# Performance work log

Measured on AMD Instinct MI355X. Metric: run time of the kernel, lower is better.

Reference implementation:

```python
import jax, jax.numpy as jnp
import numpy as np
import math

N, E, C, H = 16384, 8192, 256, 8
NNZ = 262144  # incidence pairs, avg vertex degree 16


def setup_inputs() -> dict:
    key = jax.random.key(0)
    ks = jax.random.split(key, 12)
    s = 1.0 / math.sqrt(C)
    inp = {
        "X": jax.random.normal(ks[0], (N, C), dtype=jnp.float32),
        "v_ids": jax.random.randint(ks[1], (NNZ,), 0, N, dtype=jnp.int32),
        "e_ids": jax.random.randint(ks[2], (NNZ,), 0, E, dtype=jnp.int32),
        # Linear params stored as [in, out]; y = x @ W + b  (matches torch x @ W.T + b)
        "Wq": jax.random.uniform(ks[3], (C, C), jnp.float32, -s, s),
        "bq": jax.random.uniform(ks[4], (C,), jnp.float32, -s, s),
        "Wk": jax.random.uniform(ks[5], (C, C), jnp.float32, -s, s),
        "bk": jax.random.uniform(ks[6], (C,), jnp.float32, -s, s),
        "Wv": jax.random.uniform(ks[7], (C, C), jnp.float32, -s, s),
        "bv": jax.random.uniform(ks[8], (C,), jnp.float32, -s, s),
        "Wke": jax.random.uniform(ks[9], (C, C), jnp.float32, -s, s),
        "bke": jax.random.uniform(ks[10], (C,), jnp.float32, -s, s),
    }
    return inp


def reference(X, v_ids, e_ids, Wq, bq, Wk, bk, Wv, bv, Wke, bke):
    d = C // H
    scale = 1.0 / math.sqrt(d)

    Q = (X @ Wq + bq).reshape(N, H, d)
    K = (X @ Wk + bk).reshape(N, H, d)
    V = (X @ Wv + bv).reshape(N, H, d)

    # hg.v2e_aggregation(X, 'mean'): segment-mean of incident vertex features per hyperedge
    sums = jax.ops.segment_sum(X[v_ids], e_ids, num_segments=E)          # [E, C]
    cnt = jax.ops.segment_sum(jnp.ones((NNZ,), X.dtype), e_ids, num_segments=E)
    Xe = sums / jnp.maximum(cnt, 1.0)[:, None]                            # [E, C]

    Ke = Xe @ Wke + bke                                                   # [E, C]
    Qe = X @ Wq + bq                                                      # [N, C]

    # per-node attention over heads: [N, H, H]
    attn_n = jax.nn.softmax(jnp.einsum('nhd,ngd->nhg', Q, K) * scale, axis=-1)
    X_node = jnp.einsum('nhg,ngd->nhd', attn_n, V).reshape(N, C)          # [N, C]

    # node -> hyperedge attention: [N, E]
    attn_e = jax.nn.softmax((Qe @ Ke.T) * scale, axis=-1)
    X_hyperedge = attn_e @ Xe                                             # [N, C]

    out = X_node + X_hyperedge
    # is_last=False: ReLU; bn=None; dropout in eval mode (identity)
    return jax.nn.relu(out)
```

## Files before the change

### kernel.cpp

```cpp
#include <hip/hip_runtime.h>

typedef unsigned short u16;
typedef unsigned int u32;
typedef __attribute__((ext_vector_type(4))) float f32x4;
typedef __attribute__((ext_vector_type(16))) float f32x16;
typedef __attribute__((ext_vector_type(8))) short bf16x8;
typedef __attribute__((ext_vector_type(4))) short bf16x4;
typedef __attribute__((ext_vector_type(4))) u16 u16x4;

#define N_NODES 16384
#define N_EDGES 8192
#define FK_SCALE 0.17677669529663687f
#define LOG2E 1.4426950408889634f
#define C1EXP (FK_SCALE * LOG2E)
#define NSPLIT 2

typedef const u32 __attribute__((address_space(1))) gu32;
typedef u32 __attribute__((address_space(3))) lu32;

__device__ __forceinline__ void gl_lds16(const void* g, void* l) {
  __builtin_amdgcn_global_load_lds((gu32*)g, (lu32*)l, 16, 0, 0);
}

__device__ __forceinline__ float b2f(u16 u) {
  return __builtin_bit_cast(float, (u32)u << 16);
}
__device__ __forceinline__ u16 f2b(float f) {
  u32 u = __builtin_bit_cast(u32, f);
  u += 0x7fffu + ((u >> 16) & 1u);
  return (u16)(u >> 16);
}

__global__ __launch_bounds__(256) void k_cvt(const float* __restrict__ X,
                                             u16* __restrict__ Xb) {
  int i = blockIdx.x * 256 + threadIdx.x;
  f32x4 v = *(const f32x4*)(X + i * 4);
  u16x4 r;
  r.x = f2b(v.x); r.y = f2b(v.y); r.z = f2b(v.z); r.w = f2b(v.w);
  *(u16x4*)(Xb + i * 4) = r;
}

__global__ __launch_bounds__(256) void k_wt(const float* __restrict__ Wq,
                                            const float* __restrict__ Wk,
                                            const float* __restrict__ Wv,
                                            const float* __restrict__ Wke,
                                            u16* __restrict__ Wt) {
  __shared__ float tile[64][65];
  int w = blockIdx.z;
  const float* W = (w == 0) ? Wq : (w == 1) ? Wk : (w == 2) ? Wv : Wke;
  int k0 = blockIdx.x * 64, n0 = blockIdx.y * 64;
  int tid = threadIdx.x;
#pragma unroll
  for (int i = 0; i < 16; i++) {
    int idx = i * 256 + tid;
    int kr = idx >> 6, nc = idx & 63;
    tile[nc][kr] = W[(k0 + kr) * 256 + n0 + nc];
  }
  __syncthreads();
#pragma unroll
  for (int i = 0; i < 16; i++) {
    int idx = i * 256 + tid;
    int nr = idx >> 6, kc = idx & 63;
    Wt[w * 65536 + (n0 + nr) * 256 + k0 + kc] = f2b(tile[nr][kc]);
  }
}

__global__ __launch_bounds__(256) void k_bias(const float* __restrict__ bq,
                                              const float* __restrict__ bk,
                                              const float* __restrict__ bv,
                                              const float* __restrict__ bke,
                                              float* __restrict__ bcat) {
  int i = blockIdx.x * 256 + threadIdx.x;
  float v;
  if (i < 256) v = bq[i];
  else if (i < 512) v = bk[i - 256];
  else if (i < 768) v = bv[i - 512];
  else v = bke[i - 768];
  bcat[i] = v;
}

__global__ __launch_bounds__(256) void k_hist(const int* __restrict__ e_ids,
                                              int* __restrict__ hist) {
  int base = blockIdx.x * 1024 + threadIdx.x;
#pragma unroll
  for (int k = 0; k < 4; k++) atomicAdd(&hist[e_ids[base + k * 256]], 1);
}

__global__ __launch_bounds__(256) void k_scan(const int* __restrict__ hist,
                                              int* __restrict__ eoff,
                                              int* __restrict__ cur) {
  __shared__ int ts[256];
  int t = threadIdx.x;
  int base = t * 32;
  int vals[32];
  int s = 0;
#pragma unroll
  for (int i = 0; i < 32; i++) { vals[i] = hist[base + i]; s += vals[i]; }
  ts[t] = s;
  __syncthreads();
  for (int off = 1; off < 256; off <<= 1) {
    int v = (t >= off) ? ts[t - off] : 0;
    __syncthreads();
    ts[t] += v;
    __syncthreads();
  }
  int ex = ts[t] - s;
#pragma unroll
  for (int i = 0; i < 32; i++) {
    eoff[base + i] = ex;
    cur[base + i] = ex;
    ex += vals[i];
  }
  if (t == 255) eoff[8192] = ex;
}

__global__ __launch_bounds__(256) void k_perm(const int* __restrict__ v_ids,
                                              const int* __restrict__ e_ids,
                                              int* __restrict__ cur,
                                              int* __restrict__ perm) {
  int base = blockIdx.x * 1024 + threadIdx.x;
#pragma unroll
  for (int k = 0; k < 4; k++) {
    int i = base + k * 256;
    int e = e_ids[i];
    int v = v_ids[i];
    int pos = atomicAdd(&cur[e], 1);
    perm[pos] = v;
  }
}

__global__ __launch_bounds__(256) void k_gather(const u16* __restrict__ Xb,
                                                const int* __restrict__ perm,
                                                const int* __restrict__ eoff,
                                                u16* __restrict__ Xe) {
  __shared__ float red[4][256];
  int e = blockIdx.x;
  int tid = threadIdx.x, wave = tid >> 6, lane = tid & 63;
  int start = eoff[e], end = eoff[e + 1];
  f32x4 acc = {0.f, 0.f, 0.f, 0.f};
  for (int j = start + wave; j < end; j += 4) {
    int v = perm[j];
    bf16x4 x = *(const bf16x4*)(Xb + v * 256 + lane * 4);
#pragma unroll
    for (int c = 0; c < 4; c++) acc[c] += b2f((u16)x[c]);
  }
  *(f32x4*)&red[wave][lane * 4] = acc;
  __syncthreads();
  int t = tid;
  float s = red[0][t] + red[1][t] + red[2][t] + red[3][t];
  float m = s / fmaxf((float)(end - start), 1.0f);
  Xe[e * 256 + t] = f2b(m);
}

__global__ __launch_bounds__(256) void k_xt(const u16* __restrict__ Xe,
                                            u16* __restrict__ XeTc) {
  __shared__ u16 tile[64][65];
  int e0 = blockIdx.x * 64, c0 = blockIdx.y * 64;
  int tid = threadIdx.x;
#pragma unroll
  for (int i = 0; i < 16; i++) {
    int idx = i * 256 + tid;
    int er = idx >> 6, cr = idx & 63;
    tile[cr][er] = Xe[(e0 + er) * 256 + c0 + cr];
  }
  __syncthreads();
#pragma unroll
  for (int i = 0; i < 16; i++) {
    int idx = i * 256 + tid;
    int cr = idx >> 6, er = idx & 63;
    int e = e0 + er;
    XeTc[(size_t)(e >> 3) * 2048 + (c0 + cr) * 8 + (e & 7)] = tile[cr][er];
  }
}

__global__ __launch_bounds__(256) void k_gemm64(const u16* __restrict__ A,
                                                const u16* __restrict__ Wt,
                                                const float* __restrict__ bias,
                                                u16* __restrict__ out,
                                                int ldout) {
  __shared__ u16 As[64 * 256];
  __shared__ u16 Bs[64 * 256];
  int tid = threadIdx.x;
  int mtile = blockIdx.x * 64;
  int gn = blockIdx.y * 64;
  const u16* Ap = A + mtile * 256;
  const u16* Bp = Wt + gn * 256;
#pragma unroll
  for (int i = 0; i < 8; i++) {
    gl_lds16(Ap + i * 2048 + tid * 8, As + i * 2048 + tid * 8);
    gl_lds16(Bp + i * 2048 + tid * 8, Bs + i * 2048 + tid * 8);
  }
  __syncthreads();
  int wave = tid >> 6, lane = tid & 63;
  int quad = lane >> 4, l16 = lane & 15;
  bf16x8 a[8];
#pragma unroll
  for (int kc = 0; kc < 8; kc++)
    a[kc] = *(const bf16x8*)(As + (wave * 16 + l16) * 256 + kc * 32 + quad * 8);
#pragma unroll
  for (int nt = 0; nt < 4; nt++) {
    f32x4 acc = {0.f, 0.f, 0.f, 0.f};
#pragma unroll
    for (int kc = 0; kc < 8; kc++) {
      bf16x8 b = *(const bf16x8*)(Bs + (nt * 16 + l16) * 256 + kc * 32 + quad * 8);
      acc = __builtin_amdgcn_mfma_f32_16x16x32_bf16(a[kc], b, acc, 0, 0, 0);
    }
#pragma unroll
    for (int r = 0; r < 4; r++) {
      int row = mtile + wave * 16 + quad * 4 + r;
      int col = gn + nt * 16 + l16;
      out[row * ldout + col] = f2b(acc[r] + bias[col]);
    }
  }
}

__global__ __launch_bounds__(256) void k_gemmke(const u16* __restrict__ A,
                                                const u16* __restrict__ Wt,
                                                const float* __restrict__ bias,
                                                u16* __restrict__ KebT) {
  __shared__ u16 As[64 * 256];
  __shared__ u16 Bs[64 * 256];
  int tid = threadIdx.x;
  int mtile = blockIdx.x * 64;
  int gn = blockIdx.y * 64;
  const u16* Ap = A + mtile * 256;
  const u16* Bp = Wt + gn * 256;
#pragma unroll
  for (int i = 0; i < 8; i++) {
    gl_lds16(Ap + i * 2048 + tid * 8, As + i * 2048 + tid * 8);
    gl_lds16(Bp + i * 2048 + tid * 8, Bs + i * 2048 + tid * 8);
  }
  __syncthreads();
  int wave = tid >> 6, lane = tid & 63;
  int quad = lane >> 4, l16 = lane & 15;
  bf16x8 a[8];
#pragma unroll
  for (int kc = 0; kc < 8; kc++)
    a[kc] = *(const bf16x8*)(As + (wave * 16 + l16) * 256 + kc * 32 + quad * 8);
#pragma unroll
  for (int nt = 0; nt < 4; nt++) {
    f32x4 acc = {0.f, 0.f, 0.f, 0.f};
#pragma unroll
    for (int kc = 0; kc < 8; kc++) {
      bf16x8 b = *(const bf16x8*)(Bs + (nt * 16 + l16) * 256 + kc * 32 + quad * 8);
      acc = __builtin_amdgcn_mfma_f32_16x16x32_bf16(a[kc], b, acc, 0, 0, 0);
    }
#pragma unroll
    for (int r = 0; r < 4; r++) {
      int row = mtile + wave * 16 + quad * 4 + r;
      int col = gn + nt * 16 + l16;
      KebT[(size_t)(col >> 3) * 65536 + row * 8 + (col & 7)] = f2b(acc[r] + bias[col]);
    }
  }
}

__global__ __launch_bounds__(256, 2) void k_flash(const u16* __restrict__ QKV,
                                                  const u16* __restrict__ KebT,
                                                  const u16* __restrict__ XeTc,
                                                  u16* __restrict__ Op,
                                                  float* __restrict__ Lv) {
  extern __shared__ u16 sm[];
  u16* KeL = sm;
  u16* VLT = sm + 16384;
  u16* PL = sm + 32768;
  float* lsum = (float*)(sm + 36864);
  int tid = threadIdx.x;
  int wave = tid >> 6, lane = tid & 63;
  int l31 = lane & 31, half = lane >> 5;
  int pair = wave >> 1, kh = wave & 1;
  int qt = blockIdx.x & 255;
  int split = blockIdx.x >> 8;
  int rowp0 = qt * 64 + pair * 32;
  u16* PLp = PL + pair * 2048;

  if (tid < 64) lsum[tid] = 0.f;

  bf16x8 qf[16];
#pragma unroll
  for (int ks = 0; ks < 16; ks++)
    qf[ks] = *(const bf16x8*)(QKV + (rowp0 + l31) * 768 + ks * 16 + half * 8);

  f32x16 o[4];
#pragma unroll
  for (int i = 0; i < 4; i++)
#pragma unroll
    for (int r = 0; r < 16; r++) o[i][r] = 0.f;
  float l[16];
#pragma unroll
  for (int r = 0; r < 16; r++) l[r] = 0.f;

  for (int ktl = 0; ktl < 64; ktl++) {
    int ktg = split * 64 + ktl;
    int kbase = ktg * 64;
    __syncthreads();
#pragma unroll
    for (int i = 0; i < 8; i++) {
      int s = i * 256 + tid;
      int c = s >> 6, r = s & 63;
      gl_lds16(KebT + ((size_t)c * 8192 + kbase + r) * 8, KeL + s * 8);
    }
    int kb8 = ktg * 8;
#pragma unroll
    for (int i = 0; i < 8; i++) {
      int s = i * 256 + tid;
      int kc = s >> 8, ch = s & 255;
      gl_lds16(XeTc + ((size_t)(kb8 + kc) * 256 + ch) * 8, VLT + s * 8);
    }
    __syncthreads();

    f32x16 sc;
#pragma unroll
    for (int r = 0; r < 16; r++) sc[r] = 0.f;
#pragma unroll
    for (int ks = 0; ks < 16; ks++) {
      int c = ks * 2 + half;
      bf16x8 kb = *(const bf16x8*)(KeL + c * 512 + (kh * 32 + l31) * 8);
      sc = __builtin_amdgcn_mfma_f32_32x32x16_bf16(qf[ks], kb, sc, 0, 0, 0);
    }
#pragma unroll
    for (int reg = 0; reg < 16; reg++) {
      float pv = __builtin_amdgcn_exp2f(sc[reg] * C1EXP);
      l[reg] += pv;
      int row = (reg & 3) + 8 * (reg >> 2) + 4 * half;
      int col = kh * 32 + l31;
      PLp[row * 64 + (((col >> 3) ^ (row & 7)) << 3) + (col & 7)] = f2b(pv);
    }
    __syncthreads();
    bf16x8 pf[4];
#pragma unroll
    for (int ks = 0; ks < 4; ks++) {
      int pc = ks * 2 + half;
      pf[ks] = *(const bf16x8*)(PLp + l31 * 64 + ((pc ^ (l31 & 7)) << 3));
    }
#pragma unroll
    for (int ct = 0; ct < 4; ct++) {
#pragma unroll
      for (int ks = 0; ks < 4; ks++) {
        int kc = ks * 2 + half;
        int ch = kh * 128 + ct * 32 + l31;
        bf16x8 vb = *(const bf16x8*)(VLT + kc * 2048 + ch * 8);
        o[ct] = __builtin_amdgcn_mfma_f32_32x32x16_bf16(pf[ks], vb, o[ct], 0, 0, 0);
      }
    }
  }

#pragma unroll
  for (int off = 1; off < 32; off <<= 1)
#pragma unroll
    for (int r = 0; r < 16; r++) l[r] += __shfl_xor(l[r], off, 64);
  if (l31 == 0) {
#pragma unroll
    for (int reg = 0; reg < 16; reg++) {
      int row = (reg & 3) + 8 * (reg >> 2) + 4 * half;
      atomicAdd(&lsum[pair * 32 + row], l[reg]);
    }
  }
  __syncthreads();

  size_t obase = (size_t)split * N_NODES * 256;
#pragma unroll
  for (int ct = 0; ct < 4; ct++)
#pragma unroll
    for (int reg = 0; reg < 16; reg++) {
      int row = rowp0 + (reg & 3) + 8 * (reg >> 2) + 4 * half;
      int col = kh * 128 + ct * 32 + l31;
      Op[obase + (size_t)row * 256 + col] = f2b(o[ct][reg]);
    }
  if (tid < 64) Lv[split * N_NODES + qt * 64 + tid] = lsum[tid];
}

__global__ __launch_bounds__(256) void k_comb(const u16* __restrict__ QKV,
                                              const u16* __restrict__ Op,
                                              const float* __restrict__ Lv,
                                              float* __restrict__ out) {
  int idx = blockIdx.x * 256 + threadIdx.x;
  int n = idx >> 6, lane = idx & 63;
  int h = lane >> 3, g = lane & 7;
  const u16* base = QKV + n * 768;
  const bf16x8* qp = (const bf16x8*)(base + h * 32);
  const bf16x8* kp = (const bf16x8*)(base + 256 + g * 32);
  float s = 0.f;
#pragma unroll
  for (int t = 0; t < 4; t++) {
    bf16x8 qv = qp[t], kv = kp[t];
#pragma unroll
    for (int j = 0; j < 8; j++) s += b2f((u16)qv[j]) * b2f((u16)kv[j]);
  }
  s *= FK_SCALE;
  float mx = s;
#pragma unroll
  for (int off = 1; off < 8; off <<= 1) mx = fmaxf(mx, __shfl_xor(mx, off, 64));
  float p = __builtin_amdgcn_exp2f((s - mx) * LOG2E);
  float lsum = p;
#pragma unroll
  for (int off = 1; off < 8; off <<= 1) lsum += __shfl_xor(lsum, off, 64);
  float attn = p / lsum;
  float a4[4] = {0.f, 0.f, 0.f, 0.f};
#pragma unroll
  for (int g2 = 0; g2 < 8; g2++) {
    float a = __shfl(attn, (lane & 56) | g2, 64);
    bf16x4 vv = *(const bf16x4*)(base + 512 + g2 * 32 + g * 4);
#pragma unroll
    for (int j = 0; j < 4; j++) a4[j] += a * b2f((u16)vv[j]);
  }
  int c4 = lane * 4;
  float L = 0.f;
  f32x4 acc = {0.f, 0.f, 0.f, 0.f};
#pragma unroll
  for (int sp = 0; sp < NSPLIT; sp++) {
    L += Lv[sp * N_NODES + n];
    u16x4 ov = *(const u16x4*)(Op + (size_t)sp * N_NODES * 256 + (size_t)n * 256 + c4);
    acc.x += b2f(ov.x);
    acc.y += b2f(ov.y);
    acc.z += b2f(ov.z);
    acc.w += b2f(ov.w);
  }
  float invL = 1.0f / L;
  f32x4 res;
  res.x = fmaxf(acc.x * invL + a4[0], 0.f);
  res.y = fmaxf(acc.y * invL + a4[1], 0.f);
  res.z = fmaxf(acc.z * invL + a4[2], 0.f);
  res.w = fmaxf(acc.w * invL + a4[3], 0.f);
  *(f32x4*)(out + (size_t)n * 256 + c4) = res;
}

extern "C" void kernel_launch(void* const* d_in, const int* in_sizes, int n_in,
                              void* d_out, int out_size, void* d_ws, size_t ws_size,
                              hipStream_t stream) {
  const float* X = (const float*)d_in[0];
  const int* v_ids = (const int*)d_in[1];
  const int* e_ids = (const int*)d_in[2];
  const float* Wq = (const float*)d_in[3];
  const float* bq = (const float*)d_in[4];
  const float* Wk = (const float*)d_in[5];
  const float* bk = (const float*)d_in[6];
  const float* Wv = (const float*)d_in[7];
  const float* bv = (const float*)d_in[8];
  const float* Wke = (const float*)d_in[9];
  const float* bke = (const float*)d_in[10];
  float* out = (float*)d_out;

  char* ws = (char*)d_ws;
  u16* Xb = (u16*)(ws);
  u16* QKV = (u16*)(ws + 8388608);
  u16* Wt = (u16*)(ws + 33554432);
  float* bcat = (float*)(ws + 34078720);
  int* hist = (int*)(ws + 34082816);
  int* eoff = (int*)(ws + 34115584);
  int* cur = (int*)(ws + 34152448);
  int* perm = (int*)(ws + 34185216);
  u16* Xe = (u16*)(ws + 35233792);
  u16* XeTc = (u16*)(ws + 39428096);
  u16* KebT = (u16*)(ws + 43622400);
  u16* Op = (u16*)(ws + 64593920);
  float* Lv = (float*)(ws + 98148352);

  hipMemsetAsync(hist, 0, 32768, stream);
  k_cvt<<<4096, 256, 0, stream>>>(X, Xb);
  k_wt<<<dim3(4, 4, 4), 256, 0, stream>>>(Wq, Wk, Wv, Wke, Wt);
  k_bias<<<4, 256, 0, stream>>>(bq, bk, bv, bke, bcat);
  k_hist<<<256, 256, 0, stream>>>(e_ids, hist);
  k_scan<<<1, 256, 0, stream>>>(hist, eoff, cur);
  k_perm<<<256, 256, 0, stream>>>(v_ids, e_ids, cur, perm);
  k_gather<<<8192, 256, 0, stream>>>(Xb, perm, eoff, Xe);
  k_xt<<<dim3(128, 4), 256, 0, stream>>>(Xe, XeTc);
  k_gemm64<<<dim3(256, 12), 256, 0, stream>>>(Xb, Wt, bcat, QKV, 768);
  k_gemmke<<<dim3(128, 4), 256, 0, stream>>>(Xe, Wt + 3 * 65536, bcat + 768, KebT);
  hipFuncSetAttribute((const void*)k_flash, hipFuncAttributeMaxDynamicSharedMemorySize,
                      73984);
  k_flash<<<512, 256, 73984, stream>>>(QKV, KebT, XeTc, Op, Lv);
  k_comb<<<4096, 256, 0, stream>>>(QKV, Op, Lv, out);
}
```

Before: 376.3 us.

## Fuse prep kernels, replace GEMMs with 128x128 swizzled tiles, drop LDS atomics in flash

```diff
diff --git a/kernel.cpp b/kernel.cpp
--- a/kernel.cpp
+++ b/kernel.cpp
@@ -13,7 +13,6 @@
 #define FK_SCALE 0.17677669529663687f
 #define LOG2E 1.4426950408889634f
 #define C1EXP (FK_SCALE * LOG2E)
-#define NSPLIT 2
 
 typedef const u32 __attribute__((address_space(1))) gu32;
 typedef u32 __attribute__((address_space(3))) lu32;
@@ -31,25 +30,37 @@
   return (u16)(u >> 16);
 }
 
-__global__ __launch_bounds__(256) void k_cvt(const float* __restrict__ X,
-                                             u16* __restrict__ Xb) {
+__global__ __launch_bounds__(256) void k_prep(const float* __restrict__ X,
+                                              const int* __restrict__ e_ids,
+                                              u16* __restrict__ Xb,
+                                              int* __restrict__ hist) {
   int i = blockIdx.x * 256 + threadIdx.x;
   f32x4 v = *(const f32x4*)(X + i * 4);
   u16x4 r;
   r.x = f2b(v.x); r.y = f2b(v.y); r.z = f2b(v.z); r.w = f2b(v.w);
   *(u16x4*)(Xb + i * 4) = r;
+  if (threadIdx.x < 64) atomicAdd(&hist[e_ids[blockIdx.x * 64 + threadIdx.x]], 1);
 }
 
 __global__ __launch_bounds__(256) void k_wt(const float* __restrict__ Wq,
                                             const float* __restrict__ Wk,
                                             const float* __restrict__ Wv,
                                             const float* __restrict__ Wke,
-                                            u16* __restrict__ Wt) {
+                                            const float* __restrict__ bq,
+                                            const float* __restrict__ bk,
+                                            const float* __restrict__ bv,
+                                            const float* __restrict__ bke,
+                                            u16* __restrict__ Wt,
+                                            float* __restrict__ bcat) {
   __shared__ float tile[64][65];
   int w = blockIdx.z;
   const float* W = (w == 0) ? Wq : (w == 1) ? Wk : (w == 2) ? Wv : Wke;
   int k0 = blockIdx.x * 64, n0 = blockIdx.y * 64;
   int tid = threadIdx.x;
+  if (blockIdx.x == 0 && blockIdx.y == 0) {
+    const float* b = (w == 0) ? bq : (w == 1) ? bk : (w == 2) ? bv : bke;
+    bcat[w * 256 + tid] = b[tid];
+  }
 #pragma unroll
   for (int i = 0; i < 16; i++) {
     int idx = i * 256 + tid;
@@ -63,27 +74,6 @@
     int nr = idx >> 6, kc = idx & 63;
     Wt[w * 65536 + (n0 + nr) * 256 + k0 + kc] = f2b(tile[nr][kc]);
   }
-}
-
-__global__ __launch_bounds__(256) void k_bias(const float* __restrict__ bq,
-                                              const float* __restrict__ bk,
-                                              const float* __restrict__ bv,
-                                              const float* __restrict__ bke,
-                                              float* __restrict__ bcat) {
-  int i = blockIdx.x * 256 + threadIdx.x;
-  float v;
-  if (i < 256) v = bq[i];
-  else if (i < 512) v = bk[i - 256];
-  else if (i < 768) v = bv[i - 512];
-  else v = bke[i - 768];
-  bcat[i] = v;
-}
-
-__global__ __launch_bounds__(256) void k_hist(const int* __restrict__ e_ids,
-                                              int* __restrict__ hist) {
-  int base = blockIdx.x * 1024 + threadIdx.x;
-#pragma unroll
-  for (int k = 0; k < 4; k++) atomicAdd(&hist[e_ids[base + k * 256]], 1);
 }
 
 __global__ __launch_bounds__(256) void k_scan(const int* __restrict__ hist,
@@ -132,7 +122,8 @@
 __global__ __launch_bounds__(256) void k_gather(const u16* __restrict__ Xb,
                                                 const int* __restrict__ perm,
                                                 const int* __restrict__ eoff,
-                                                u16* __restrict__ Xe) {
+                                                u16* __restrict__ Xe,
+                                                u16* __restrict__ XeTc) {
   __shared__ float red[4][256];
   int e = blockIdx.x;
   int tid = threadIdx.x, wave = tid >> 6, lane = tid & 63;
@@ -149,109 +140,80 @@
   int t = tid;
   float s = red[0][t] + red[1][t] + red[2][t] + red[3][t];
   float m = s / fmaxf((float)(end - start), 1.0f);
-  Xe[e * 256 + t] = f2b(m);
-}
-
-__global__ __launch_bounds__(256) void k_xt(const u16* __restrict__ Xe,
-                                            u16* __restrict__ XeTc) {
-  __shared__ u16 tile[64][65];
-  int e0 = blockIdx.x * 64, c0 = blockIdx.y * 64;
+  u16 b = f2b(m);
+  Xe[e * 256 + t] = b;
+  XeTc[(size_t)(e >> 3) * 2048 + t * 8 + (e & 7)] = b;
+}
+
+__global__ __launch_bounds__(256) void k_gemm128(const u16* __restrict__ A,
+                                                 const u16* __restrict__ Wt,
+                                                 const float* __restrict__ bias,
+                                                 u16* __restrict__ out,
+                                                 int ldout, int tmode) {
+  __shared__ u16 As[128 * 64];
+  __shared__ u16 Bs[128 * 64];
   int tid = threadIdx.x;
-#pragma unroll
-  for (int i = 0; i < 16; i++) {
-    int idx = i * 256 + tid;
-    int er = idx >> 6, cr = idx & 63;
-    tile[cr][er] = Xe[(e0 + er) * 256 + c0 + cr];
-  }
-  __syncthreads();
-#pragma unroll
-  for (int i = 0; i < 16; i++) {
-    int idx = i * 256 + tid;
-    int cr = idx >> 6, er = idx & 63;
-    int e = e0 + er;
-    XeTc[(size_t)(e >> 3) * 2048 + (c0 + cr) * 8 + (e & 7)] = tile[cr][er];
-  }
-}
-
-__global__ __launch_bounds__(256) void k_gemm64(const u16* __restrict__ A,
-                                                const u16* __restrict__ Wt,
-                                                const float* __restrict__ bias,
-                                                u16* __restrict__ out,
-                                                int ldout) {
-  __shared__ u16 As[64 * 256];
-  __shared__ u16 Bs[64 * 256];
-  int tid = threadIdx.x;
-  int mtile = blockIdx.x * 64;
-  int gn = blockIdx.y * 64;
-  const u16* Ap = A + mtile * 256;
-  const u16* Bp = Wt + gn * 256;
-#pragma unroll
-  for (int i = 0; i < 8; i++) {
-    gl_lds16(Ap + i * 2048 + tid * 8, As + i * 2048 + tid * 8);
-    gl_lds16(Bp + i * 2048 + tid * 8, Bs + i * 2048 + tid * 8);
-  }
-  __syncthreads();
   int wave = tid >> 6, lane = tid & 63;
   int quad = lane >> 4, l16 = lane & 15;
-  bf16x8 a[8];
-#pragma unroll
-  for (int kc = 0; kc < 8; kc++)
-    a[kc] = *(const bf16x8*)(As + (wave * 16 + l16) * 256 + kc * 32 + quad * 8);
-#pragma unroll
-  for (int nt = 0; nt < 4; nt++) {
-    f32x4 acc = {0.f, 0.f, 0.f, 0.f};
-#pragma unroll
-    for (int kc = 0; kc < 8; kc++) {
-      bf16x8 b = *(const bf16x8*)(Bs + (nt * 16 + l16) * 256 + kc * 32 + quad * 8);
-      acc = __builtin_amdgcn_mfma_f32_16x16x32_bf16(a[kc], b, acc, 0, 0, 0);
-    }
-#pragma unroll
-    for (int r = 0; r < 4; r++) {
-      int row = mtile + wave * 16 + quad * 4 + r;
-      int col = gn + nt * 16 + l16;
-      out[row * ldout + col] = f2b(acc[r] + bias[col]);
-    }
-  }
-}
-
-__global__ __launch_bounds__(256) void k_gemmke(const u16* __restrict__ A,
-                                                const u16* __restrict__ Wt,
-                                                const float* __restrict__ bias,
-                                                u16* __restrict__ KebT) {
-  __shared__ u16 As[64 * 256];
-  __shared__ u16 Bs[64 * 256];
-  int tid = threadIdx.x;
-  int mtile = blockIdx.x * 64;
-  int gn = blockIdx.y * 64;
-  const u16* Ap = A + mtile * 256;
-  const u16* Bp = Wt + gn * 256;
-#pragma unroll
-  for (int i = 0; i < 8; i++) {
-    gl_lds16(Ap + i * 2048 + tid * 8, As + i * 2048 + tid * 8);
-    gl_lds16(Bp + i * 2048 + tid * 8, Bs + i * 2048 + tid * 8);
-  }
-  __syncthreads();
-  int wave = tid >> 6, lane = tid & 63;
-  int quad = lane >> 4, l16 = lane & 15;
-  bf16x8 a[8];
-#pragma unroll
-  for (int kc = 0; kc < 8; kc++)
-    a[kc] = *(const bf16x8*)(As + (wave * 16 + l16) * 256 + kc * 32 + quad * 8);
-#pragma unroll
-  for (int nt = 0; nt < 4; nt++) {
-    f32x4 acc = {0.f, 0.f, 0.f, 0.f};
-#pragma unroll
-    for (int kc = 0; kc < 8; kc++) {
-      bf16x8 b = *(const bf16x8*)(Bs + (nt * 16 + l16) * 256 + kc * 32 + quad * 8);
-      acc = __builtin_amdgcn_mfma_f32_16x16x32_bf16(a[kc], b, acc, 0, 0, 0);
-    }
-#pragma unroll
-    for (int r = 0; r < 4; r++) {
-      int row = mtile + wave * 16 + quad * 4 + r;
-      int col = gn + nt * 16 + l16;
-      KebT[(size_t)(col >> 3) * 65536 + row * 8 + (col & 7)] = f2b(acc[r] + bias[col]);
-    }
-  }
+  int wm = wave >> 1, wn = wave & 1;
+  int mtile = blockIdx.x * 128, ntile = blockIdx.y * 128;
+  const u16* Ap = A + (size_t)mtile * 256;
+  const u16* Bp = Wt + (size_t)ntile * 256;
+
+  f32x4 acc[4][4];
+#pragma unroll
+  for (int am = 0; am < 4; am++)
+#pragma unroll
+    for (int bn = 0; bn < 4; bn++) acc[am][bn] = (f32x4){0.f, 0.f, 0.f, 0.f};
+
+  for (int ks = 0; ks < 4; ks++) {
+    __syncthreads();
+#pragma unroll
+    for (int i = 0; i < 4; i++) {
+      int s = i * 256 + tid;
+      int r = s >> 3, c = s & 7;
+      gl_lds16(Ap + r * 256 + ks * 64 + ((c ^ (r & 7)) << 3), As + s * 8);
+    }
+#pragma unroll
+    for (int i = 0; i < 4; i++) {
+      int s = i * 256 + tid;
+      int r = s >> 3, c = s & 7;
+      gl_lds16(Bp + r * 256 + ks * 64 + ((c ^ (r & 7)) << 3), Bs + s * 8);
+    }
+    __syncthreads();
+#pragma unroll
+    for (int kc = 0; kc < 2; kc++) {
+      bf16x8 a[4], b[4];
+      int cc = kc * 4 + quad;
+#pragma unroll
+      for (int am = 0; am < 4; am++) {
+        int rl = wm * 64 + am * 16 + l16;
+        a[am] = *(const bf16x8*)(As + rl * 64 + ((cc ^ (rl & 7)) << 3));
+      }
+#pragma unroll
+      for (int bn = 0; bn < 4; bn++) {
+        int rl = wn * 64 + bn * 16 + l16;
+        b[bn] = *(const bf16x8*)(Bs + rl * 64 + ((cc ^ (rl & 7)) << 3));
+      }
+#pragma unroll
+      for (int am = 0; am < 4; am++)
+#pragma unroll
+        for (int bn = 0; bn < 4; bn++)
+          acc[am][bn] = __builtin_amdgcn_mfma_f32_16x16x32_bf16(a[am], b[bn], acc[am][bn], 0, 0, 0);
+    }
+  }
+#pragma unroll
+  for (int am = 0; am < 4; am++)
+#pragma unroll
+    for (int bn = 0; bn < 4; bn++)
+#pragma unroll
+      for (int r = 0; r < 4; r++) {
+        int row = mtile + wm * 64 + am * 16 + quad * 4 + r;
+        int col = ntile + wn * 64 + bn * 16 + l16;
+        u16 v = f2b(acc[am][bn][r] + bias[col]);
+        if (tmode == 0) out[(size_t)row * ldout + col] = v;
+        else out[(size_t)(col >> 3) * 65536 + row * 8 + (col & 7)] = v;
+      }
 }
 
 __global__ __launch_bounds__(256, 2) void k_flash(const u16* __restrict__ QKV,
@@ -263,7 +225,6 @@
   u16* KeL = sm;
   u16* VLT = sm + 16384;
   u16* PL = sm + 32768;
-  float* lsum = (float*)(sm + 36864);
   int tid = threadIdx.x;
   int wave = tid >> 6, lane = tid & 63;
   int l31 = lane & 31, half = lane >> 5;
@@ -273,8 +234,6 @@
   int rowp0 = qt * 64 + pair * 32;
   u16* PLp = PL + pair * 2048;
 
-  if (tid < 64) lsum[tid] = 0.f;
-
   bf16x8 qf[16];
 #pragma unroll
   for (int ks = 0; ks < 16; ks++)
@@ -352,10 +311,9 @@
 #pragma unroll
     for (int reg = 0; reg < 16; reg++) {
       int row = (reg & 3) + 8 * (reg >> 2) + 4 * half;
-      atomicAdd(&lsum[pair * 32 + row], l[reg]);
-    }
-  }
-  __syncthreads();
+      Lv[(split * 2 + kh) * N_NODES + rowp0 + row] = l[reg];
+    }
+  }
 
   size_t obase = (size_t)split * N_NODES * 256;
 #pragma unroll
@@ -366,7 +324,6 @@
       int col = kh * 128 + ct * 32 + l31;
       Op[obase + (size_t)row * 256 + col] = f2b(o[ct][reg]);
     }
-  if (tid < 64) Lv[split * N_NODES + qt * 64 + tid] = lsum[tid];
 }
 
 __global__ __launch_bounds__(256) void k_comb(const u16* __restrict__ QKV,
@@ -405,10 +362,11 @@
   }
   int c4 = lane * 4;
   float L = 0.f;
+#pragma unroll
+  for (int sl = 0; sl < 4; sl++) L += Lv[sl * N_NODES + n];
   f32x4 acc = {0.f, 0.f, 0.f, 0.f};
 #pragma unroll
-  for (int sp = 0; sp < NSPLIT; sp++) {
-    L += Lv[sp * N_NODES + n];
+  for (int sp = 0; sp < 2; sp++) {
     u16x4 ov = *(const u16x4*)(Op + (size_t)sp * N_NODES * 256 + (size_t)n * 256 + c4);
     acc.x += b2f(ov.x);
     acc.y += b2f(ov.y);
@@ -456,18 +414,15 @@
   float* Lv = (float*)(ws + 98148352);
 
   hipMemsetAsync(hist, 0, 32768, stream);
-  k_cvt<<<4096, 256, 0, stream>>>(X, Xb);
-  k_wt<<<dim3(4, 4, 4), 256, 0, stream>>>(Wq, Wk, Wv, Wke, Wt);
-  k_bias<<<4, 256, 0, stream>>>(bq, bk, bv, bke, bcat);
-  k_hist<<<256, 256, 0, stream>>>(e_ids, hist);
+  k_prep<<<4096, 256, 0, stream>>>(X, e_ids, Xb, hist);
+  k_wt<<<dim3(4, 4, 4), 256, 0, stream>>>(Wq, Wk, Wv, Wke, bq, bk, bv, bke, Wt, bcat);
   k_scan<<<1, 256, 0, stream>>>(hist, eoff, cur);
   k_perm<<<256, 256, 0, stream>>>(v_ids, e_ids, cur, perm);
-  k_gather<<<8192, 256, 0, stream>>>(Xb, perm, eoff, Xe);
-  k_xt<<<dim3(128, 4), 256, 0, stream>>>(Xe, XeTc);
-  k_gemm64<<<dim3(256, 12), 256, 0, stream>>>(Xb, Wt, bcat, QKV, 768);
-  k_gemmke<<<dim3(128, 4), 256, 0, stream>>>(Xe, Wt + 3 * 65536, bcat + 768, KebT);
+  k_gather<<<8192, 256, 0, stream>>>(Xb, perm, eoff, Xe, XeTc);
+  k_gemm128<<<dim3(128, 6), 256, 0, stream>>>(Xb, Wt, bcat, QKV, 768, 0);
+  k_gemm128<<<dim3(64, 2), 256, 0, stream>>>(Xe, Wt + 3 * 65536, bcat + 768, KebT, 0, 1);
   hipFuncSetAttribute((const void*)k_flash, hipFuncAttributeMaxDynamicSharedMemorySize,
-                      73984);
-  k_flash<<<512, 256, 73984, stream>>>(QKV, KebT, XeTc, Op, Lv);
+                      73728);
+  k_flash<<<512, 256, 73728, stream>>>(QKV, KebT, XeTc, Op, Lv);
   k_comb<<<4096, 256, 0, stream>>>(QKV, Op, Lv, out);
 }
```

Measured after the change: 366.8 us. 1.03x faster.
